# Optimization experiments

Hardware: AMD Instinct MI355X
Metric: run time of the kernel (lower is better)

Reference implementation:

```python
import jax, jax.numpy as jnp
import numpy as np

D = 256      # d_model
H = 8        # nhead
HD = D // H  # head_dim
B = 16       # ragged batch size
L = 4096     # tokens per sample (equal lengths here; code handles general ragged)
NQ = 100     # instance queries per sample


def _xavier(key, shape):
    a = float(np.sqrt(6.0 / (shape[0] + shape[1])))
    return jax.random.uniform(key, shape, jnp.float32, -a, a)


def setup_inputs() -> dict:
    key = jax.random.key(0)
    ks = jax.random.split(key, 8)
    total = B * L
    source = jax.random.normal(ks[0], (total, D), jnp.float32)
    query = jax.random.normal(ks[1], (B, NQ, D), jnp.float32)
    batch_offsets = (jnp.arange(B + 1) * L).astype(jnp.int32)
    # nn.MultiheadAttention params: in-proj (split into q/k/v) + out-proj.
    Wq = _xavier(ks[2], (D, D)); bq = jnp.zeros((D,), jnp.float32)
    Wk = _xavier(ks[3], (D, D)); bk = jnp.zeros((D,), jnp.float32)
    Wv = _xavier(ks[4], (D, D)); bv = jnp.zeros((D,), jnp.float32)
    Wo = _xavier(ks[5], (D, D)); bo = jnp.zeros((D,), jnp.float32)
    return {"source": source, "query": query, "batch_offsets": batch_offsets,
            "Wq": Wq, "bq": bq, "Wk": Wk, "bk": bk, "Wv": Wv, "bv": bv,
            "Wo": Wo, "bo": bo}


def reference(source, query, batch_offsets, Wq, bq, Wk, bk, Wv, bv, Wo, bo):
    # Ragged -> padded gather (indices are concrete, computed with numpy).
    offs = np.asarray(batch_offsets)
    lens = offs[1:] - offs[:-1]                      # (B,)
    Lmax = int(lens.max())
    pos = np.arange(Lmax)
    mask = pos[None, :] < lens[:, None]              # (B, Lmax) valid keys
    idx = np.where(mask, offs[:-1, None] + pos[None, :], 0)
    kv_in = source[jnp.asarray(idx)]                 # (B, Lmax, D)

    # Projections (torch Linear: x @ W.T + b), split into heads.
    q = (query @ Wq.T + bq).reshape(B, NQ, H, HD)
    k = (kv_in @ Wk.T + bk).reshape(B, Lmax, H, HD)
    v = (kv_in @ Wv.T + bv).reshape(B, Lmax, H, HD)

    scale = 1.0 / jnp.sqrt(jnp.asarray(HD, q.dtype))
    scores = jnp.einsum("bqhd,bkhd->bhqk", q * scale, k)
    scores = jnp.where(jnp.asarray(mask)[:, None, None, :], scores, -1e30)
    attn = jax.nn.softmax(scores, axis=-1)           # (B, H, NQ, Lmax)
    ctx = jnp.einsum("bhqk,bkhd->bqhd", attn, v).reshape(B, NQ, D)
    out = ctx @ Wo.T + bo
    # Original code: dropout/norm results are discarded; residual add of query.
    return out + query
```

## Files before the change

kernel.cpp:

```cpp
#include <hip/hip_runtime.h>
#include <hip/hip_bf16.h>
#include <math.h>

#define DM     256
#define NHEAD  8
#define HDIM   32
#define QPAD   112
#define NCHUNK 8
#define BM     64
#define BN     256
#define BK     32
#define ALD    264
#define QR     4
#define CQ     4

typedef __attribute__((ext_vector_type(8))) short bf16x8;
typedef __attribute__((ext_vector_type(4))) short bf16x4;
typedef __attribute__((ext_vector_type(4))) float f32x4;

__device__ __forceinline__ short f2bf(float f) {
  union { float f; unsigned u; } x; x.f = f;
  unsigned u = (x.u + 0x7fffu + ((x.u >> 16) & 1u)) >> 16;
  return (short)u;
}
__device__ __forceinline__ float bf2f(short s) {
  union { unsigned u; float f; } x; x.u = ((unsigned)(unsigned short)s) << 16;
  return x.f;
}
__device__ __forceinline__ bf16x8 bzero8() {
  bf16x8 v;
#pragma unroll
  for (int j = 0; j < 8; j++) v[j] = (short)0;
  return v;
}
__device__ __forceinline__ bf16x8 cvt8(const float* p) {
  float4 x0 = *(const float4*)p, x1 = *(const float4*)(p + 4);
  bf16x8 v;
  v[0] = f2bf(x0.x); v[1] = f2bf(x0.y); v[2] = f2bf(x0.z); v[3] = f2bf(x0.w);
  v[4] = f2bf(x1.x); v[5] = f2bf(x1.y); v[6] = f2bf(x1.z); v[7] = f2bf(x1.w);
  return v;
}

__global__ __launch_bounds__(256) void wconv_kernel(
    const float* __restrict__ Wk, const float* __restrict__ Wv,
    short* __restrict__ Wkv) {
  int idx = blockIdx.x * 256 + threadIdx.x;
  int e0 = idx * 8;
  const float* p = (e0 < DM * DM) ? (Wk + e0) : (Wv + (e0 - DM * DM));
  *(bf16x8*)(Wkv + e0) = cvt8(p);
}

__global__ __launch_bounds__(256) void q_proj_kernel(
    const float* __restrict__ query, const float* __restrict__ Wq,
    const float* __restrict__ bq, short* __restrict__ Qw, int Bn, int NQ) {
  int b  = blockIdx.x / (QPAD / QR);
  int r0 = (blockIdx.x % (QPAD / QR)) * QR;
  __shared__ __align__(16) float ql[QR * DM];
  int tid = threadIdx.x;
  for (int i = tid; i < QR * DM; i += 256) {
    int r = r0 + (i >> 8);
    ql[i] = (r < NQ) ? query[((size_t)b * NQ + r) * DM + (i & 255)] : 0.f;
  }
  __syncthreads();
  int d = tid;
  float bias = bq[d];
  float acc[QR];
#pragma unroll
  for (int qi = 0; qi < QR; qi++) acc[qi] = bias;
  const float* wrow = Wq + (size_t)d * DM;
  for (int k = 0; k < DM; k += 4) {
    float4 w = *(const float4*)(wrow + k);
#pragma unroll
    for (int qi = 0; qi < QR; qi++) {
      float4 x = *(const float4*)&ql[qi * DM + k];
      acc[qi] += x.x * w.x + x.y * w.y + x.z * w.z + x.w * w.w;
    }
  }
  const float scale = 0.17677669529663687f;
  int h = d >> 5, hd = d & 31;
#pragma unroll
  for (int qi = 0; qi < QR; qi++) {
    int r = r0 + qi;
    float v = (r < NQ) ? acc[qi] * scale : 0.f;
    Qw[(((size_t)b * NHEAD + h) * QPAD + r) * HDIM + hd] = f2bf(v);
  }
}

__global__ __launch_bounds__(256) void kv_gemm_kernel(
    const float* __restrict__ src, const short* __restrict__ Wkv,
    const float* __restrict__ bk, const float* __restrict__ bv,
    const int* __restrict__ offs, short* __restrict__ Kw,
    short* __restrict__ Vw, int T, int Bn, int Mtiles) {
  int bid = blockIdx.x;
  int mtile = (bid >> 4) * 8 + (bid & 7);
  int ntile = (bid >> 3) & 1;
  if (mtile >= Mtiles) return;
  int t0 = mtile * BM;
  int n0 = ntile * BN;
  bool isK = (ntile == 0);
  const float* bias = isK ? bk : bv;

  int tid = threadIdx.x;
  int wave = tid >> 6, lane = tid & 63;
  int l15 = lane & 15, quad = lane >> 4;

  __shared__ __align__(16) short As[BM * ALD];

  f32x4 acc[4][4];
#pragma unroll
  for (int i = 0; i < 4; i++)
#pragma unroll
    for (int j = 0; j < 4; j++) acc[i][j] = (f32x4){0.f, 0.f, 0.f, 0.f};

  {
    int arow = tid >> 2, ac4 = tid & 3;
    int atok = t0 + arow;
    if (atok >= T) atok = T - 1;
    const float* arp = src + (size_t)atok * DM;
#pragma unroll
    for (int r = 0; r < 4; r++) {
      int c0 = r * 64 + ac4 * 16;
      const float* p = arp + c0;
      bf16x8 v0 = cvt8(p);
      bf16x8 v1 = cvt8(p + 8);
      *(bf16x8*)&As[arow * ALD + c0]     = v0;
      *(bf16x8*)&As[arow * ALD + c0 + 8] = v1;
    }
  }
  __syncthreads();

  const short* bptr = Wkv + (size_t)(n0 + wave * 64 + l15) * DM + quad * 8;
#pragma unroll
  for (int kk = 0; kk < DM; kk += BK) {
    bf16x8 bf_[4];
#pragma unroll
    for (int nt = 0; nt < 4; nt++)
      bf_[nt] = *(const bf16x8*)(bptr + (size_t)nt * 16 * DM + kk);
    bf16x8 af[4];
#pragma unroll
    for (int mt = 0; mt < 4; mt++)
      af[mt] = *(const bf16x8*)&As[(mt * 16 + l15) * ALD + kk + quad * 8];
    if (isK) {
#pragma unroll
      for (int mt = 0; mt < 4; mt++)
#pragma unroll
        for (int nt = 0; nt < 4; nt++)
          acc[mt][nt] = __builtin_amdgcn_mfma_f32_16x16x32_bf16(
              bf_[nt], af[mt], acc[mt][nt], 0, 0, 0);
    } else {
#pragma unroll
      for (int mt = 0; mt < 4; mt++)
#pragma unroll
        for (int nt = 0; nt < 4; nt++)
          acc[mt][nt] = __builtin_amdgcn_mfma_f32_16x16x32_bf16(
              af[mt], bf_[nt], acc[mt][nt], 0, 0, 0);
    }
  }

  if (isK) {
    float bk4[4][4];
    int hK[4], hdK[4];
#pragma unroll
    for (int nt = 0; nt < 4; nt++) {
      int nbq = wave * 64 + nt * 16 + quad * 4;
      float4 b4 = *(const float4*)(bias + nbq);
      bk4[nt][0] = b4.x; bk4[nt][1] = b4.y; bk4[nt][2] = b4.z; bk4[nt][3] = b4.w;
      hK[nt] = nbq >> 5;
      hdK[nt] = nbq & 31;
    }
    int bcur = 0;
#pragma unroll
    for (int mt = 0; mt < 4; mt++) {
      int tok = t0 + mt * 16 + l15;
      if (tok >= T) continue;
      while (bcur + 1 < Bn && offs[bcur + 1] <= tok) bcur++;
      int off = offs[bcur], len = offs[bcur + 1] - off;
      int l = tok - off;
      size_t bb = (size_t)off * DM;
#pragma unroll
      for (int nt = 0; nt < 4; nt++) {
        bf16x4 p;
#pragma unroll
        for (int r = 0; r < 4; r++) p[r] = f2bf(acc[mt][nt][r] + bk4[nt][r]);
        *(bf16x4*)&Kw[bb + (size_t)hK[nt] * len * HDIM + (size_t)l * HDIM +
                      hdK[nt]] = p;
      }
    }
  } else {
    float bV[4];
    int hV[4], hdV[4];
#pragma unroll
    for (int nt = 0; nt < 4; nt++) {
      int nb = wave * 64 + nt * 16 + l15;
      bV[nt] = bias[nb];
      hV[nt] = nb >> 5;
      hdV[nt] = nb & 31;
    }
    int bcur = 0;
#pragma unroll
    for (int mt = 0; mt < 4; mt++) {
      int tb = t0 + mt * 16 + quad * 4;
      if (tb >= T) continue;
      while (bcur + 1 < Bn && offs[bcur + 1] <= tb) bcur++;
      int off = offs[bcur], len = offs[bcur + 1] - off;
      size_t bb = (size_t)off * DM;
      bool span = (tb + 3 < offs[bcur + 1]) && (tb + 3 < T);
      if (span) {
        int l = tb - off;
#pragma unroll
        for (int nt = 0; nt < 4; nt++) {
          size_t idx =
              bb + (size_t)hV[nt] * len * HDIM + (size_t)hdV[nt] * len + l;
          bf16x4 p;
#pragma unroll
          for (int r = 0; r < 4; r++) p[r] = f2bf(acc[mt][nt][r] + bV[nt]);
          if ((idx & 3) == 0) {
            *(bf16x4*)&Vw[idx] = p;
          } else {
#pragma unroll
            for (int r = 0; r < 4; r++) Vw[idx + r] = p[r];
          }
        }
      } else {
        int bc2 = bcur;
#pragma unroll
        for (int r = 0; r < 4; r++) {
          int tok = tb + r;
          if (tok >= T) continue;
          while (bc2 + 1 < Bn && offs[bc2 + 1] <= tok) bc2++;
          int off2 = offs[bc2], len2 = offs[bc2 + 1] - off2;
          int l = tok - off2;
          size_t bb2 = (size_t)off2 * DM;
#pragma unroll
          for (int nt = 0; nt < 4; nt++)
            Vw[bb2 + (size_t)hV[nt] * len2 * HDIM + (size_t)hdV[nt] * len2 +
               l] = f2bf(acc[mt][nt][r] + bV[nt]);
        }
      }
    }
  }
}

__global__ __launch_bounds__(448) void attn_kernel(
    const short* __restrict__ Qw, const short* __restrict__ Kw,
    const short* __restrict__ Vw, const int* __restrict__ offs,
    short* __restrict__ Ops, float* __restrict__ Ml, int Bn) {
  int c  = blockIdx.x % NCHUNK;
  int bh = blockIdx.x / NCHUNK;
  int h = bh % NHEAD, b = bh / NHEAD;
  int wave = threadIdx.x >> 6, lane = threadIdx.x & 63;
  int l15 = lane & 15, quad = lane >> 4;

  int off = offs[b], len = offs[b + 1] - off;
  int cl = ((len + NCHUNK * 32 - 1) / (NCHUNK * 32)) * 32;
  int kstart = c * cl;
  int kend   = min(kstart + cl, len);

  const short* Kh = Kw + (size_t)off * DM + (size_t)h * len * HDIM;
  const short* Vh = Vw + (size_t)off * DM + (size_t)h * len * HDIM;

  int row16 = wave * 16 + l15;
  bf16x8 aq = *(const bf16x8*)(
      Qw + (((size_t)b * NHEAD + h) * QPAD + row16) * HDIM + quad * 8);

  f32x4 o[2];
#pragma unroll
  for (int j = 0; j < 2; j++) o[j] = (f32x4){0.f, 0.f, 0.f, 0.f};
  float mrun[4], lrun[4];
#pragma unroll
  for (int r = 0; r < 4; r++) { mrun[r] = -1e30f; lrun[r] = 0.f; }

  __shared__ __align__(16) short plds[7][16][40];

  for (int kb = kstart; kb < kend; kb += 32) {
    bool valid[2];
    bf16x8 bk_[2];
#pragma unroll
    for (int nt = 0; nt < 2; nt++) {
      int key = kb + nt * 16 + l15;
      valid[nt] = key < kend;
      bk_[nt] = valid[nt]
                    ? *(const bf16x8*)(Kh + (size_t)key * HDIM + quad * 8)
                    : bzero8();
    }
    f32x4 zero = {0.f, 0.f, 0.f, 0.f};
    f32x4 s[2];
#pragma unroll
    for (int nt = 0; nt < 2; nt++)
      s[nt] = __builtin_amdgcn_mfma_f32_16x16x32_bf16(aq, bk_[nt], zero, 0, 0, 0);
#pragma unroll
    for (int r = 0; r < 4; r++) {
      float v0 = valid[0] ? s[0][r] : -1e30f;
      float v1 = valid[1] ? s[1][r] : -1e30f;
      float t = fmaxf(v0, v1);
      t = fmaxf(t, __shfl_xor(t, 1, 16));
      t = fmaxf(t, __shfl_xor(t, 2, 16));
      t = fmaxf(t, __shfl_xor(t, 4, 16));
      t = fmaxf(t, __shfl_xor(t, 8, 16));
      float mn = fmaxf(mrun[r], t);
      float al = __expf(mrun[r] - mn);
      float p0 = valid[0] ? __expf(v0 - mn) : 0.f;
      float p1 = valid[1] ? __expf(v1 - mn) : 0.f;
      float rs = p0 + p1;
      rs += __shfl_xor(rs, 1, 16);
      rs += __shfl_xor(rs, 2, 16);
      rs += __shfl_xor(rs, 4, 16);
      rs += __shfl_xor(rs, 8, 16);
      lrun[r] = al * lrun[r] + rs;
      mrun[r] = mn;
      o[0][r] *= al;
      o[1][r] *= al;
      plds[wave][quad * 4 + r][l15]      = f2bf(p0);
      plds[wave][quad * 4 + r][16 + l15] = f2bf(p1);
    }
    bf16x8 pa = *(const bf16x8*)&plds[wave][l15][quad * 8];
    bf16x8 bv_[2];
#pragma unroll
    for (int ht = 0; ht < 2; ht++) {
      int hd = ht * 16 + l15;
      int k0 = kb + quad * 8;
      const short* p = Vh + (size_t)hd * len + k0;
      if (k0 + 7 < len) {
        bv_[ht] = *(const bf16x8*)p;
      } else {
        bf16x8 v;
#pragma unroll
        for (int j = 0; j < 8; j++) v[j] = (k0 + j < len) ? p[j] : (short)0;
        bv_[ht] = v;
      }
    }
#pragma unroll
    for (int ht = 0; ht < 2; ht++)
      o[ht] = __builtin_amdgcn_mfma_f32_16x16x32_bf16(pa, bv_[ht], o[ht], 0, 0, 0);
  }

#pragma unroll
  for (int r = 0; r < 4; r++) {
    int row = wave * 16 + quad * 4 + r;
    size_t base = (((size_t)c * Bn + b) * NHEAD + h) * QPAD + row;
#pragma unroll
    for (int ht = 0; ht < 2; ht++)
      Ops[base * HDIM + ht * 16 + l15] = f2bf(o[ht][r]);
    if (l15 == 0) {
      Ml[base * 2]     = mrun[r];
      Ml[base * 2 + 1] = lrun[r];
    }
  }
}

__global__ __launch_bounds__(256) void combine_kernel(
    const short* __restrict__ Ops, const float* __restrict__ Ml,
    const float* __restrict__ query, const float* __restrict__ Wo,
    const float* __restrict__ bo, float* __restrict__ out, int Bn, int NQ) {
  int bpb = (NQ + CQ - 1) / CQ;
  int b  = blockIdx.x / bpb;
  int q0 = (blockIdx.x % bpb) * CQ;
  int tid = threadIdx.x;

  __shared__ __align__(16) short opsl[CQ][NCHUNK][DM];
  __shared__ float mll[NCHUNK][NHEAD][CQ][2];
  __shared__ __align__(16) float ctx[CQ * DM];

  for (int t = tid; t < CQ * NCHUNK * (DM / 8); t += 256) {
    int q   = t / (NCHUNK * 32);
    int rem = t % (NCHUNK * 32);
    int c   = rem / 32;
    int v   = rem % 32;
    int h   = v >> 2;
    int hd0 = (v & 3) * 8;
    int qq = q0 + q;
    if (qq >= NQ) qq = NQ - 1;
    size_t base = (((size_t)c * Bn + b) * NHEAD + h) * QPAD + qq;
    *(bf16x8*)&opsl[q][c][v * 8] = *(const bf16x8*)&Ops[base * HDIM + hd0];
  }
  for (int t = tid; t < CQ * NCHUNK * NHEAD; t += 256) {
    int q   = t / (NCHUNK * NHEAD);
    int rem = t % (NCHUNK * NHEAD);
    int c   = rem / NHEAD;
    int h   = rem % NHEAD;
    int qq = q0 + q;
    if (qq >= NQ) qq = NQ - 1;
    size_t base = (((size_t)c * Bn + b) * NHEAD + h) * QPAD + qq;
    mll[c][h][q][0] = Ml[base * 2];
    mll[c][h][q][1] = Ml[base * 2 + 1];
  }
  __syncthreads();

  int d = tid, h = d >> 5;
#pragma unroll
  for (int qi = 0; qi < CQ; qi++) {
    float M = -1e30f;
#pragma unroll
    for (int c = 0; c < NCHUNK; c++) M = fmaxf(M, mll[c][h][qi][0]);
    float L = 0.f, acc = 0.f;
#pragma unroll
    for (int c = 0; c < NCHUNK; c++) {
      float w = __expf(mll[c][h][qi][0] - M);
      L += mll[c][h][qi][1] * w;
      acc += w * bf2f(opsl[qi][c][d]);
    }
    ctx[qi * DM + d] = (L > 0.f) ? acc / L : 0.f;
  }
  __syncthreads();

  const float* wrow = Wo + (size_t)d * DM;
  float acc[CQ];
  float bias = bo[d];
#pragma unroll
  for (int qi = 0; qi < CQ; qi++) acc[qi] = bias;
  for (int k = 0; k < DM; k += 4) {
    float4 w = *(const float4*)(wrow + k);
#pragma unroll
    for (int qi = 0; qi < CQ; qi++) {
      float4 x = *(const float4*)&ctx[qi * DM + k];
      acc[qi] += x.x * w.x + x.y * w.y + x.z * w.z + x.w * w.w;
    }
  }
#pragma unroll
  for (int qi = 0; qi < CQ; qi++) {
    int q = q0 + qi;
    if (q < NQ)
      out[((size_t)b * NQ + q) * DM + d] =
          acc[qi] + query[((size_t)b * NQ + q) * DM + d];
  }
}

extern "C" void kernel_launch(void* const* d_in, const int* in_sizes, int n_in,
                              void* d_out, int out_size, void* d_ws,
                              size_t ws_size, hipStream_t stream) {
  const float* src   = (const float*)d_in[0];
  const float* query = (const float*)d_in[1];
  const int*   offs  = (const int*)d_in[2];
  const float* Wq = (const float*)d_in[3];
  const float* bq = (const float*)d_in[4];
  const float* Wk = (const float*)d_in[5];
  const float* bk = (const float*)d_in[6];
  const float* Wv = (const float*)d_in[7];
  const float* bv = (const float*)d_in[8];
  const float* Wo = (const float*)d_in[9];
  const float* bo = (const float*)d_in[10];
  float* out = (float*)d_out;

  int T  = in_sizes[0] / DM;
  int Bn = in_sizes[2] - 1;
  int NQ = in_sizes[1] / (Bn * DM);

  char* w = (char*)d_ws;
  size_t qsz = (size_t)Bn * NHEAD * QPAD * HDIM * 2;
  size_t ksz = (size_t)T * DM * 2;
  size_t osz = (size_t)NCHUNK * Bn * NHEAD * QPAD * HDIM * 2;
  size_t msz = (size_t)NCHUNK * Bn * NHEAD * QPAD * 2 * 4;
  short* Qw  = (short*)w;
  short* Kw  = (short*)(w + qsz);
  short* Vw  = (short*)(w + qsz + ksz);
  short* Ops = (short*)(w + qsz + 2 * ksz);
  float* Mlp = (float*)(w + qsz + 2 * ksz + osz);
  short* Wkv = (short*)(w + qsz + 2 * ksz + osz + msz);

  int Mtiles = (T + BM - 1) / BM;
  int groups = (Mtiles + 7) / 8;

  wconv_kernel<<<(2 * DM * DM) / (256 * 8), 256, 0, stream>>>(Wk, Wv, Wkv);
  q_proj_kernel<<<Bn * (QPAD / QR), 256, 0, stream>>>(query, Wq, bq, Qw, Bn,
                                                      NQ);
  kv_gemm_kernel<<<groups * 16, 256, 0, stream>>>(
      src, Wkv, bk, bv, offs, Kw, Vw, T, Bn, Mtiles);
  attn_kernel<<<Bn * NHEAD * NCHUNK, 448, 0, stream>>>(Qw, Kw, Vw, offs, Ops,
                                                       Mlp, Bn);
  combine_kernel<<<Bn * ((NQ + CQ - 1) / CQ), 256, 0, stream>>>(
      Ops, Mlp, query, Wo, bo, out, Bn, NQ);
}
```

Baseline: 256.4 us.

## Fuse Q/KV projection kernels, convert weights inline, widen attention key step to 64

Merges the weight-conversion, Q-projection and KV GEMM kernels into one launch, where the first blocks handle Q rows and the rest do the KV GEMM. The GEMM now reads the fp32 Wk/Wv directly and converts to bf16 in registers instead of using a pre-converted copy. Separately, the attention loop processes 64 keys per iteration instead of 32, halving the number of online-softmax reductions and rescales per key. The trade-offs are redundant fp32 weight loads and conversions in every GEMM block, plus higher register and LDS use in the attention kernel.

Measured after the change: 271.5 us. +5.9%, slower.

```diff
diff --git a/kernel.cpp b/kernel.cpp
--- a/kernel.cpp
+++ b/kernel.cpp
@@ -41,70 +41,62 @@
   return v;
 }
 
-__global__ __launch_bounds__(256) void wconv_kernel(
-    const float* __restrict__ Wk, const float* __restrict__ Wv,
-    short* __restrict__ Wkv) {
-  int idx = blockIdx.x * 256 + threadIdx.x;
-  int e0 = idx * 8;
-  const float* p = (e0 < DM * DM) ? (Wk + e0) : (Wv + (e0 - DM * DM));
-  *(bf16x8*)(Wkv + e0) = cvt8(p);
-}
-
-__global__ __launch_bounds__(256) void q_proj_kernel(
-    const float* __restrict__ query, const float* __restrict__ Wq,
-    const float* __restrict__ bq, short* __restrict__ Qw, int Bn, int NQ) {
-  int b  = blockIdx.x / (QPAD / QR);
-  int r0 = (blockIdx.x % (QPAD / QR)) * QR;
+__global__ __launch_bounds__(256) void kvq_kernel(
+    const float* __restrict__ src, const float* __restrict__ query,
+    const float* __restrict__ Wq, const float* __restrict__ bq,
+    const float* __restrict__ Wk, const float* __restrict__ bk,
+    const float* __restrict__ Wv, const float* __restrict__ bv,
+    const int* __restrict__ offs, short* __restrict__ Qw,
+    short* __restrict__ Kw, short* __restrict__ Vw, int T, int Bn, int NQ,
+    int Mtiles, int nqb) {
+  __shared__ __align__(16) short As[BM * ALD];
   __shared__ __align__(16) float ql[QR * DM];
   int tid = threadIdx.x;
-  for (int i = tid; i < QR * DM; i += 256) {
-    int r = r0 + (i >> 8);
-    ql[i] = (r < NQ) ? query[((size_t)b * NQ + r) * DM + (i & 255)] : 0.f;
-  }
-  __syncthreads();
-  int d = tid;
-  float bias = bq[d];
-  float acc[QR];
-#pragma unroll
-  for (int qi = 0; qi < QR; qi++) acc[qi] = bias;
-  const float* wrow = Wq + (size_t)d * DM;
-  for (int k = 0; k < DM; k += 4) {
-    float4 w = *(const float4*)(wrow + k);
+
+  if (blockIdx.x < (unsigned)nqb) {
+    int b  = blockIdx.x / (QPAD / QR);
+    int r0 = (blockIdx.x % (QPAD / QR)) * QR;
+    for (int i = tid; i < QR * DM; i += 256) {
+      int r = r0 + (i >> 8);
+      ql[i] = (r < NQ) ? query[((size_t)b * NQ + r) * DM + (i & 255)] : 0.f;
+    }
+    __syncthreads();
+    int d = tid;
+    float bias = bq[d];
+    float acc[QR];
+#pragma unroll
+    for (int qi = 0; qi < QR; qi++) acc[qi] = bias;
+    const float* wrow = Wq + (size_t)d * DM;
+    for (int k = 0; k < DM; k += 4) {
+      float4 w = *(const float4*)(wrow + k);
+#pragma unroll
+      for (int qi = 0; qi < QR; qi++) {
+        float4 x = *(const float4*)&ql[qi * DM + k];
+        acc[qi] += x.x * w.x + x.y * w.y + x.z * w.z + x.w * w.w;
+      }
+    }
+    const float scale = 0.17677669529663687f;
+    int h = d >> 5, hd = d & 31;
 #pragma unroll
     for (int qi = 0; qi < QR; qi++) {
-      float4 x = *(const float4*)&ql[qi * DM + k];
-      acc[qi] += x.x * w.x + x.y * w.y + x.z * w.z + x.w * w.w;
-    }
-  }
-  const float scale = 0.17677669529663687f;
-  int h = d >> 5, hd = d & 31;
-#pragma unroll
-  for (int qi = 0; qi < QR; qi++) {
-    int r = r0 + qi;
-    float v = (r < NQ) ? acc[qi] * scale : 0.f;
-    Qw[(((size_t)b * NHEAD + h) * QPAD + r) * HDIM + hd] = f2bf(v);
-  }
-}
-
-__global__ __launch_bounds__(256) void kv_gemm_kernel(
-    const float* __restrict__ src, const short* __restrict__ Wkv,
-    const float* __restrict__ bk, const float* __restrict__ bv,
-    const int* __restrict__ offs, short* __restrict__ Kw,
-    short* __restrict__ Vw, int T, int Bn, int Mtiles) {
-  int bid = blockIdx.x;
+      int r = r0 + qi;
+      float v = (r < NQ) ? acc[qi] * scale : 0.f;
+      Qw[(((size_t)b * NHEAD + h) * QPAD + r) * HDIM + hd] = f2bf(v);
+    }
+    return;
+  }
+
+  int bid = blockIdx.x - nqb;
   int mtile = (bid >> 4) * 8 + (bid & 7);
   int ntile = (bid >> 3) & 1;
   if (mtile >= Mtiles) return;
   int t0 = mtile * BM;
-  int n0 = ntile * BN;
   bool isK = (ntile == 0);
   const float* bias = isK ? bk : bv;
-
-  int tid = threadIdx.x;
+  const float* Wsel = isK ? Wk : Wv;
+
   int wave = tid >> 6, lane = tid & 63;
   int l15 = lane & 15, quad = lane >> 4;
-
-  __shared__ __align__(16) short As[BM * ALD];
 
   f32x4 acc[4][4];
 #pragma unroll
@@ -129,13 +121,13 @@
   }
   __syncthreads();
 
-  const short* bptr = Wkv + (size_t)(n0 + wave * 64 + l15) * DM + quad * 8;
+  const float* bptrf = Wsel + (size_t)(wave * 64 + l15) * DM + quad * 8;
 #pragma unroll
   for (int kk = 0; kk < DM; kk += BK) {
     bf16x8 bf_[4];
 #pragma unroll
     for (int nt = 0; nt < 4; nt++)
-      bf_[nt] = *(const bf16x8*)(bptr + (size_t)nt * 16 * DM + kk);
+      bf_[nt] = cvt8(bptrf + (size_t)nt * 16 * DM + kk);
     bf16x8 af[4];
 #pragma unroll
     for (int mt = 0; mt < 4; mt++)
@@ -270,13 +262,13 @@
 #pragma unroll
   for (int r = 0; r < 4; r++) { mrun[r] = -1e30f; lrun[r] = 0.f; }
 
-  __shared__ __align__(16) short plds[7][16][40];
-
-  for (int kb = kstart; kb < kend; kb += 32) {
-    bool valid[2];
-    bf16x8 bk_[2];
-#pragma unroll
-    for (int nt = 0; nt < 2; nt++) {
+  __shared__ __align__(16) short plds[7][16][72];
+
+  for (int kb = kstart; kb < kend; kb += 64) {
+    bool valid[4];
+    bf16x8 bk_[4];
+#pragma unroll
+    for (int nt = 0; nt < 4; nt++) {
       int key = kb + nt * 16 + l15;
       valid[nt] = key < kend;
       bk_[nt] = valid[nt]
@@ -284,15 +276,17 @@
                     : bzero8();
     }
     f32x4 zero = {0.f, 0.f, 0.f, 0.f};
-    f32x4 s[2];
-#pragma unroll
-    for (int nt = 0; nt < 2; nt++)
+    f32x4 s[4];
+#pragma unroll
+    for (int nt = 0; nt < 4; nt++)
       s[nt] = __builtin_amdgcn_mfma_f32_16x16x32_bf16(aq, bk_[nt], zero, 0, 0, 0);
 #pragma unroll
     for (int r = 0; r < 4; r++) {
       float v0 = valid[0] ? s[0][r] : -1e30f;
       float v1 = valid[1] ? s[1][r] : -1e30f;
-      float t = fmaxf(v0, v1);
+      float v2 = valid[2] ? s[2][r] : -1e30f;
+      float v3 = valid[3] ? s[3][r] : -1e30f;
+      float t = fmaxf(fmaxf(v0, v1), fmaxf(v2, v3));
       t = fmaxf(t, __shfl_xor(t, 1, 16));
       t = fmaxf(t, __shfl_xor(t, 2, 16));
       t = fmaxf(t, __shfl_xor(t, 4, 16));
@@ -301,7 +295,9 @@
       float al = __expf(mrun[r] - mn);
       float p0 = valid[0] ? __expf(v0 - mn) : 0.f;
       float p1 = valid[1] ? __expf(v1 - mn) : 0.f;
-      float rs = p0 + p1;
+      float p2 = valid[2] ? __expf(v2 - mn) : 0.f;
+      float p3 = valid[3] ? __expf(v3 - mn) : 0.f;
+      float rs = (p0 + p1) + (p2 + p3);
       rs += __shfl_xor(rs, 1, 16);
       rs += __shfl_xor(rs, 2, 16);
       rs += __shfl_xor(rs, 4, 16);
@@ -312,26 +308,36 @@
       o[1][r] *= al;
       plds[wave][quad * 4 + r][l15]      = f2bf(p0);
       plds[wave][quad * 4 + r][16 + l15] = f2bf(p1);
-    }
-    bf16x8 pa = *(const bf16x8*)&plds[wave][l15][quad * 8];
-    bf16x8 bv_[2];
+      plds[wave][quad * 4 + r][32 + l15] = f2bf(p2);
+      plds[wave][quad * 4 + r][48 + l15] = f2bf(p3);
+    }
+    bf16x8 pa0 = *(const bf16x8*)&plds[wave][l15][quad * 8];
+    bf16x8 pa1 = *(const bf16x8*)&plds[wave][l15][32 + quad * 8];
+    bf16x8 bv_[2][2];
+#pragma unroll
+    for (int half = 0; half < 2; half++) {
+#pragma unroll
+      for (int ht = 0; ht < 2; ht++) {
+        int hd = ht * 16 + l15;
+        int k0 = kb + half * 32 + quad * 8;
+        const short* p = Vh + (size_t)hd * len + k0;
+        if (k0 + 7 < len) {
+          bv_[half][ht] = *(const bf16x8*)p;
+        } else {
+          bf16x8 v;
+#pragma unroll
+          for (int j = 0; j < 8; j++) v[j] = (k0 + j < len) ? p[j] : (short)0;
+          bv_[half][ht] = v;
+        }
+      }
+    }
 #pragma unroll
     for (int ht = 0; ht < 2; ht++) {
-      int hd = ht * 16 + l15;
-      int k0 = kb + quad * 8;
-      const short* p = Vh + (size_t)hd * len + k0;
-      if (k0 + 7 < len) {
-        bv_[ht] = *(const bf16x8*)p;
-      } else {
-        bf16x8 v;
-#pragma unroll
-        for (int j = 0; j < 8; j++) v[j] = (k0 + j < len) ? p[j] : (short)0;
-        bv_[ht] = v;
-      }
-    }
-#pragma unroll
-    for (int ht = 0; ht < 2; ht++)
-      o[ht] = __builtin_amdgcn_mfma_f32_16x16x32_bf16(pa, bv_[ht], o[ht], 0, 0, 0);
+      o[ht] = __builtin_amdgcn_mfma_f32_16x16x32_bf16(pa0, bv_[0][ht], o[ht],
+                                                      0, 0, 0);
+      o[ht] = __builtin_amdgcn_mfma_f32_16x16x32_bf16(pa1, bv_[1][ht], o[ht],
+                                                      0, 0, 0);
+    }
   }
 
 #pragma unroll
@@ -449,22 +455,19 @@
   size_t qsz = (size_t)Bn * NHEAD * QPAD * HDIM * 2;
   size_t ksz = (size_t)T * DM * 2;
   size_t osz = (size_t)NCHUNK * Bn * NHEAD * QPAD * HDIM * 2;
-  size_t msz = (size_t)NCHUNK * Bn * NHEAD * QPAD * 2 * 4;
   short* Qw  = (short*)w;
   short* Kw  = (short*)(w + qsz);
   short* Vw  = (short*)(w + qsz + ksz);
   short* Ops = (short*)(w + qsz + 2 * ksz);
   float* Mlp = (float*)(w + qsz + 2 * ksz + osz);
-  short* Wkv = (short*)(w + qsz + 2 * ksz + osz + msz);
 
   int Mtiles = (T + BM - 1) / BM;
   int groups = (Mtiles + 7) / 8;
-
-  wconv_kernel<<<(2 * DM * DM) / (256 * 8), 256, 0, stream>>>(Wk, Wv, Wkv);
-  q_proj_kernel<<<Bn * (QPAD / QR), 256, 0, stream>>>(query, Wq, bq, Qw, Bn,
-                                                      NQ);
-  kv_gemm_kernel<<<groups * 16, 256, 0, stream>>>(
-      src, Wkv, bk, bv, offs, Kw, Vw, T, Bn, Mtiles);
+  int nqb = Bn * (QPAD / QR);
+
+  kvq_kernel<<<nqb + groups * 16, 256, 0, stream>>>(
+      src, query, Wq, bq, Wk, bk, Wv, bv, offs, Qw, Kw, Vw, T, Bn, NQ, Mtiles,
+      nqb);
   attn_kernel<<<Bn * NHEAD * NCHUNK, 448, 0, stream>>>(Qw, Kw, Vw, offs, Ops,
                                                        Mlp, Bn);
   combine_kernel<<<Bn * ((NQ + CQ - 1) / CQ), 256, 0, stream>>>(
```
